# Performance work log

Measured on AMD Instinct MI355X. Metric: run time of the kernel, lower is better.

Reference implementation:

```python
import jax, jax.numpy as jnp
import numpy as np
from jax import lax

DIM = 1024
D_STATE = 64
D_CONV = 4
EXPAND = 2
HEADDIM = 64
D_INNER = EXPAND * DIM            # 2048
NHEADS = D_INNER // HEADDIM       # 32
NGROUPS = 1
CONV_DIM = D_INNER + 2 * NGROUPS * D_STATE      # 2176
D_IN_PROJ = 2 * D_INNER + 2 * NGROUPS * D_STATE + NHEADS  # 4256
BATCH, SEQLEN = 2, 4096
EPS = 1e-5


def setup_inputs() -> dict:
    key = jax.random.key(0)
    ks = jax.random.split(key, 10)
    X = jax.random.normal(ks[0], (BATCH, SEQLEN, DIM), dtype=jnp.float32)
    in_proj_w = jax.random.normal(ks[1], (D_IN_PROJ, DIM), dtype=jnp.float32) * 0.02
    conv_w = jax.random.normal(ks[2], (CONV_DIM, 1, D_CONV), dtype=jnp.float32) * 0.2
    conv_b = jax.random.normal(ks[3], (CONV_DIM,), dtype=jnp.float32) * 0.02
    dt_bias = jax.random.normal(ks[4], (NHEADS,), dtype=jnp.float32) * 0.5 - 2.0
    A_log = jnp.log(jax.random.uniform(ks[5], (NHEADS,), minval=1.0, maxval=16.0))
    D = jax.random.normal(ks[6], (NHEADS,), dtype=jnp.float32)
    norm_w = jnp.ones((D_INNER,), dtype=jnp.float32)
    out_proj_w = jax.random.normal(ks[7], (DIM, D_INNER), dtype=jnp.float32) * 0.02
    to_h_w = jax.random.normal(ks[8], (2 * DIM, DIM), dtype=jnp.float32) * 0.02
    return dict(X=X, in_proj_w=in_proj_w, conv_w=conv_w, conv_b=conv_b,
                dt_bias=dt_bias, A_log=A_log, D=D, norm_w=norm_w,
                out_proj_w=out_proj_w, to_h_w=to_h_w)


def _silu(x):
    return x * jax.nn.sigmoid(x)


def _mamba2(X, in_proj_w, conv_w, conv_b, dt_bias, A_log, D, norm_w, out_proj_w):
    Bsz, L, _ = X.shape
    zxbcdt = jnp.einsum('bld,ed->ble', X, in_proj_w)  # (B,L,D_IN_PROJ)
    z = zxbcdt[..., :D_INNER]
    xBC = zxbcdt[..., D_INNER:D_INNER + CONV_DIM]
    dt_raw = zxbcdt[..., D_INNER + CONV_DIM:]
    dt = jax.nn.softplus(dt_raw + dt_bias)  # (B,L,H)

    # causal depthwise conv over time, then silu
    xc = jnp.transpose(xBC, (0, 2, 1))                       # (B,C,L)
    xc = jnp.pad(xc, ((0, 0), (0, 0), (D_CONV - 1, 0)))
    xc = lax.conv_general_dilated(xc, conv_w, window_strides=(1,), padding='VALID',
                                  dimension_numbers=('NCH', 'OIH', 'NCH'),
                                  feature_group_count=CONV_DIM)
    xc = xc + conv_b[None, :, None]
    xBC = _silu(jnp.transpose(xc, (0, 2, 1)))                # (B,L,C)

    x = xBC[..., :D_INNER].reshape(Bsz, L, NHEADS, HEADDIM)  # (B,L,H,P)
    Bm = xBC[..., D_INNER:D_INNER + D_STATE]                 # (B,L,N) ngroups=1
    Cm = xBC[..., D_INNER + D_STATE:]                        # (B,L,N)

    A = -jnp.exp(A_log)                                      # (H,)

    def step(h, inp):
        dt_t, B_t, C_t, x_t = inp   # (B,H), (B,N), (B,N), (B,H,P)
        dA = jnp.exp(dt_t * A)                               # (B,H)
        h = h * dA[..., None, None] + jnp.einsum('bh,bhp,bn->bhpn', dt_t, x_t, B_t)
        y_t = jnp.einsum('bhpn,bn->bhp', h, C_t)
        return h, y_t

    h0 = jnp.zeros((Bsz, NHEADS, HEADDIM, D_STATE), dtype=X.dtype)
    xs = (jnp.moveaxis(dt, 1, 0), jnp.moveaxis(Bm, 1, 0),
          jnp.moveaxis(Cm, 1, 0), jnp.moveaxis(x, 1, 0))
    _, ys = lax.scan(step, h0, xs)                           # (L,B,H,P)
    y = jnp.moveaxis(ys, 0, 1) + x * D[None, None, :, None]  # skip term
    y = y.reshape(Bsz, L, D_INNER)

    # gated RMSNorm: rmsnorm(y * silu(z)) * weight
    y = y * _silu(z)
    y = y * lax.rsqrt(jnp.mean(y * y, axis=-1, keepdims=True) + EPS) * norm_w
    return jnp.einsum('bld,ed->ble', y, out_proj_w)          # (B,L,DIM)


def reference(X, in_proj_w, conv_w, conv_b, dt_bias, A_log, D, norm_w, out_proj_w, to_h_w):
    H = _mamba2(X, in_proj_w, conv_w, conv_b, dt_bias, A_log, D, norm_w, out_proj_w)
    HKV = jnp.einsum('bld,ed->ble', H, to_h_w)               # (B,L,2*DIM)
    HK, HV = HKV[..., :DIM], HKV[..., DIM:]
    return (HK, HV)
```

## Files before the change

### kernel.cpp

```cpp
#include <hip/hip_runtime.h>
#include <hip/hip_bf16.h>
#include <math.h>

#define B_       2
#define L_       4096
#define DIM_     1024
#define DINNER_  2048
#define DSTATE_  64
#define NH_      32
#define HD_      64
#define CONVDIM_ 2176
#define DIP_     4256
#define M_       (B_*L_)
#define XRW_     2208
#define NC_      64

typedef __attribute__((ext_vector_type(8))) short short8;
typedef __attribute__((ext_vector_type(4))) float floatx4;
typedef __hip_bfloat16 bf16;

__device__ __forceinline__ float bf2f(unsigned short u) {
    unsigned int v = ((unsigned int)u) << 16;
    return __builtin_bit_cast(float, v);
}
__device__ __forceinline__ unsigned short f2bf(float f) {
    unsigned int x = __builtin_bit_cast(unsigned int, f);
    unsigned int lsb = (x >> 16) & 1u;
    x += 0x7fffu + lsb;
    return (unsigned short)(x >> 16);
}
__device__ __forceinline__ void storeo(bf16* p, float v) {
    *reinterpret_cast<unsigned short*>(p) = f2bf(v);
}
__device__ __forceinline__ void storeo(float* p, float v) { *p = v; }

__device__ __forceinline__ void gl2lds16(const bf16* g, short* lds) {
    __builtin_amdgcn_global_load_lds(
        (const __attribute__((address_space(1))) void*)g,
        (__attribute__((address_space(3))) void*)lds, 16, 0, 0);
}

__global__ __launch_bounds__(256) void cast_f32_bf16_k(
    const float* __restrict__ src, bf16* __restrict__ dst)
{
    size_t i0 = ((size_t)blockIdx.x * 256 + threadIdx.x) * 8;
    uint4 a = *reinterpret_cast<const uint4*>(src + i0);
    uint4 b = *reinterpret_cast<const uint4*>(src + i0 + 4);
    unsigned int w0 = (unsigned int)f2bf(__builtin_bit_cast(float, a.x)) |
                      ((unsigned int)f2bf(__builtin_bit_cast(float, a.y)) << 16);
    unsigned int w1 = (unsigned int)f2bf(__builtin_bit_cast(float, a.z)) |
                      ((unsigned int)f2bf(__builtin_bit_cast(float, a.w)) << 16);
    unsigned int w2 = (unsigned int)f2bf(__builtin_bit_cast(float, b.x)) |
                      ((unsigned int)f2bf(__builtin_bit_cast(float, b.y)) << 16);
    unsigned int w3 = (unsigned int)f2bf(__builtin_bit_cast(float, b.z)) |
                      ((unsigned int)f2bf(__builtin_bit_cast(float, b.w)) << 16);
    *reinterpret_cast<uint4*>(reinterpret_cast<unsigned short*>(dst) + i0) =
        make_uint4(w0, w1, w2, w3);
}

template <typename TO>
__global__ __launch_bounds__(512, 2) void gemm256(
    const bf16* __restrict__ Ag, const bf16* __restrict__ Wg,
    TO* __restrict__ outA, TO* __restrict__ outB,
    int M, int N, int K, int split, int strideA, int strideB, int nbx)
{
    __shared__ short lds[65536];

    const int tid  = threadIdx.x;
    const int wave = tid >> 6;
    const int lane = tid & 63;
    const int ln   = lane & 15;
    const int quad = lane >> 4;
    const int wr   = wave >> 2;
    const int wc   = wave & 3;
    const int bh   = wc >> 1;
    const int wcl  = wc & 1;
    const int xorv = (ln & 7) << 4;

    int nwg  = gridDim.x;
    int orig = blockIdx.x;
    int wg   = ((nwg & 7) == 0) ? ((orig & 7) * (nwg >> 3) + (orig >> 3)) : orig;
    const int bx = wg % nbx;
    const int by = wg / nbx;
    const int m0 = by * 256;
    const int n0 = bx * 256;

    int lo0 = tid * 16;
    int lo1 = 8192 + tid * 16;
    int so0 = lo0 ^ (((lo0 >> 7) & 7) << 4);
    int so1 = lo1 ^ (((lo1 >> 7) & 7) << 4);
    const int srow0 = so0 >> 7, scol0 = (so0 & 127) >> 1;
    const int srow1 = so1 >> 7, scol1 = (so1 & 127) >> 1;

#define STG_A(bufb, h, kc) do {                                               \
    short* dst_ = &lds[((bufb)*2 + (h)) * 8192 + wave * 512];                 \
    gl2lds16(Ag + (size_t)(m0 + (h)*128 + srow0) * K + (kc) + scol0, dst_);   \
    gl2lds16(Ag + (size_t)(m0 + (h)*128 + srow1) * K + (kc) + scol1, dst_ + 4096); \
} while (0)
#define STG_B(bufb, h, kc) do {                                               \
    short* dst_ = &lds[32768 + ((bufb)*2 + (h)) * 8192 + wave * 512];         \
    gl2lds16(Wg + (size_t)(n0 + (h)*128 + srow0) * K + (kc) + scol0, dst_);   \
    gl2lds16(Wg + (size_t)(n0 + (h)*128 + srow1) * K + (kc) + scol1, dst_ + 4096); \
} while (0)

#define RD_A(qi) do {                                                         \
    const char* Ab_ = (const char*)&lds[(cur*2 + wr) * 8192];                 \
    _Pragma("unroll") for (int i = 0; i < 4; i++)                             \
    _Pragma("unroll") for (int ks = 0; ks < 2; ks++)                          \
        af[i][ks] = *reinterpret_cast<const short8*>(                         \
            Ab_ + ((((qi)*64 + i*16 + ln)*128 + ks*64 + quad*16) ^ xorv));    \
} while (0)
#define RD_B(qj, BV) do {                                                     \
    const char* Bb_ = (const char*)&lds[32768 + (cur*2 + bh) * 8192];         \
    _Pragma("unroll") for (int j = 0; j < 2; j++)                             \
    _Pragma("unroll") for (int ks = 0; ks < 2; ks++)                          \
        BV[j][ks] = *reinterpret_cast<const short8*>(                         \
            Bb_ + (((wcl*64 + (qj)*32 + j*16 + ln)*128 + ks*64 + quad*16) ^ xorv)); \
} while (0)

#define MMA(qi, qj, BV) do {                                                  \
    _Pragma("unroll") for (int i = 0; i < 4; i++)                             \
    _Pragma("unroll") for (int j = 0; j < 2; j++)                             \
    _Pragma("unroll") for (int ks = 0; ks < 2; ks++)                          \
        acc[(qi)*4+i][(qj)*2+j] = __builtin_amdgcn_mfma_f32_16x16x32_bf16(    \
            af[i][ks], BV[j][ks], acc[(qi)*4+i][(qj)*2+j], 0, 0, 0);          \
} while (0)

    floatx4 acc[8][4];
#pragma unroll
    for (int i = 0; i < 8; i++)
#pragma unroll
        for (int j = 0; j < 4; j++) acc[i][j] = (floatx4){0.f, 0.f, 0.f, 0.f};

    const int NT = K >> 6;

    STG_A(0, 0, 0); STG_A(0, 1, 0);
    STG_B(0, 0, 0); STG_B(0, 1, 0);
    asm volatile("s_waitcnt vmcnt(0)" ::: "memory");
    __builtin_amdgcn_s_barrier();
    __builtin_amdgcn_sched_barrier(0);

    short8 af[4][2], bf0[2][2], bf1[2][2];

    for (int t = 0; t < NT; ++t) {
        const int cur = t & 1, nxt = cur ^ 1;
        const int kc  = (t + 1) << 6;
        const bool pf = (t + 1 < NT);

        RD_A(0);
        RD_B(0, bf0);
        RD_B(1, bf1);

        if (pf) {
            STG_A(nxt, 0, kc); STG_A(nxt, 1, kc);
            STG_B(nxt, 0, kc); STG_B(nxt, 1, kc);
        }

        __builtin_amdgcn_s_setprio(1);
        MMA(0, 0, bf0);
        MMA(0, 1, bf1);
        RD_A(1);
        MMA(1, 1, bf1);
        MMA(1, 0, bf0);
        __builtin_amdgcn_s_setprio(0);

        if (pf) { asm volatile("s_waitcnt vmcnt(0)" ::: "memory"); }
        __builtin_amdgcn_s_barrier();
        __builtin_amdgcn_sched_barrier(0);
    }

#undef STG_A
#undef STG_B
#undef RD_A
#undef RD_B
#undef MMA

#pragma unroll
    for (int qi = 0; qi < 2; qi++)
#pragma unroll
    for (int i = 0; i < 4; i++)
#pragma unroll
    for (int qj = 0; qj < 2; qj++)
#pragma unroll
    for (int j = 0; j < 2; j++)
#pragma unroll
    for (int r = 0; r < 4; r++) {
        int grow = m0 + wr*128 + qi*64 + i*16 + quad*4 + r;
        int gcol = n0 + wc*64 + qj*32 + j*16 + ln;
        float v = acc[qi*4+i][qj*2+j][r];
        if (gcol < N) {
            if (gcol < split)
                storeo(outA + (size_t)grow * strideA + gcol, v);
            else
                storeo(outB + (size_t)grow * strideB + (gcol - split), v);
        }
    }
}

__global__ __launch_bounds__(256) void conv_all_k(
    const bf16* __restrict__ xr, const float* __restrict__ cw,
    const float* __restrict__ cb, bf16* __restrict__ xc)
{
    int idx = blockIdx.x * 256 + threadIdx.x;
    int row = idx / 272;
    int ch0 = (idx - row * 272) * 8;
    int t   = row & (L_ - 1);
    const unsigned short* xru = (const unsigned short*)xr;
    uint4 rv[4];
#pragma unroll
    for (int j = 0; j < 4; j++) {
        rv[j] = make_uint4(0u, 0u, 0u, 0u);
        if (t + j - 3 >= 0)
            rv[j] = *reinterpret_cast<const uint4*>(xru + (size_t)(row + j - 3) * XRW_ + ch0);
    }
    unsigned int ow[4];
#pragma unroll
    for (int pair = 0; pair < 4; pair++) {
        unsigned short o2[2];
#pragma unroll
        for (int k = 0; k < 2; k++) {
            int cc = pair * 2 + k;
            float a = cb[ch0 + cc];
#pragma unroll
            for (int j = 0; j < 4; j++) {
                unsigned int w32 = (&rv[j].x)[cc >> 1];
                unsigned short u = (cc & 1) ? (unsigned short)(w32 >> 16)
                                            : (unsigned short)(w32 & 0xffffu);
                a = fmaf(bf2f(u), cw[(ch0 + cc) * 4 + j], a);
            }
            o2[k] = f2bf(a / (1.f + __expf(-a)));
        }
        ow[pair] = (unsigned int)o2[0] | ((unsigned int)o2[1] << 16);
    }
    *reinterpret_cast<uint4*>((unsigned short*)xc + (size_t)row * CONVDIM_ + ch0) =
        make_uint4(ow[0], ow[1], ow[2], ow[3]);
}

__global__ __launch_bounds__(256) void dt_k(
    const bf16* __restrict__ xr, const float* __restrict__ dtb, float* __restrict__ dtf)
{
    int idx = blockIdx.x * 256 + threadIdx.x;
    int h  = idx & (NH_ - 1);
    int ml = idx >> 5;
    float v = bf2f(((const unsigned short*)xr)[(size_t)ml * XRW_ + 2176 + h]) + dtb[h];
    dtf[idx] = fmaxf(v, 0.f) + log1pf(__expf(-fabsf(v)));
}

__global__ __launch_bounds__(256) void chunk_intra_k(
    const bf16* __restrict__ xc, const float* __restrict__ dtf,
    const float* __restrict__ A_log, const float* __restrict__ Dp,
    bf16* __restrict__ Yg, float* __restrict__ Sg, float* __restrict__ Eg)
{
    __shared__ short Bst[64*72];
    __shared__ short Cst[64*72];
    __shared__ short xsM[64*72];
    __shared__ short xT [64*72];
    __shared__ short BwT[64*72];
    __shared__ float dts[64], cums[64], wS[64];

    const int tid  = threadIdx.x;
    const int bid  = blockIdx.x;
    const int h    = bid & 31;
    const int bc   = bid >> 5;
    const int c    = bc & 63;
    const int b    = bc >> 6;
    const int xch0 = h * 64;
    const unsigned short* xcu = (const unsigned short*)xc;

    const float Ah = -__expf(A_log[h]);
    const float Dh = Dp[h];

    for (int q = tid; q < 1536; q += 256) {
        int sel = q >> 9;
        int qq  = q & 511;
        int r = qq >> 3, c8 = (qq & 7) * 8;
        size_t ro = (size_t)(b * L_ + c * 64 + r) * CONVDIM_;
        if (sel == 0)
            *reinterpret_cast<uint4*>(&Bst[r*72 + c8]) =
                *reinterpret_cast<const uint4*>(xcu + ro + 2048 + c8);
        else if (sel == 1)
            *reinterpret_cast<uint4*>(&Cst[r*72 + c8]) =
                *reinterpret_cast<const uint4*>(xcu + ro + 2112 + c8);
        else
            *reinterpret_cast<uint4*>(&xsM[r*72 + c8]) =
                *reinterpret_cast<const uint4*>(xcu + ro + xch0 + c8);
    }
    if (tid < 64) dts[tid] = dtf[(size_t)(b * L_ + c * 64 + tid) * NH_ + h];
    __syncthreads();

    if (tid == 0) {
        float cc = 0.f;
        for (int t = 0; t < 64; t++) { cc += dts[t] * Ah; cums[t] = cc; }
    }
    __syncthreads();
    if (tid < 64) wS[tid] = __expf(cums[63] - cums[tid]) * dts[tid];
    if (tid == 0) Eg[bid] = __expf(cums[63]);
    __syncthreads();

    for (int q = tid; q < 4096; q += 256) {
        int s = q & 63, ch = q >> 6;
        xT [ch*72 + s] = xsM[s*72 + ch];
        BwT[ch*72 + s] = (short)f2bf(bf2f((unsigned short)Bst[s*72 + ch]) * wS[s]);
    }
    __syncthreads();

    const int wave = tid >> 6, lane = tid & 63;
    const int ln = lane & 15, quad = lane >> 4;
    const int wm = (wave >> 1) * 32, wn = (wave & 1) * 32;

    floatx4 accG[2][2];
#pragma unroll
    for (int i = 0; i < 2; i++)
#pragma unroll
        for (int j = 0; j < 2; j++) accG[i][j] = (floatx4){0.f,0.f,0.f,0.f};
#pragma unroll
    for (int kk = 0; kk < 64; kk += 32) {
        short8 af[2], bfv[2];
#pragma unroll
        for (int i = 0; i < 2; i++)
            af[i] = *reinterpret_cast<const short8*>(&Cst[(wm + i*16 + ln)*72 + kk + quad*8]);
#pragma unroll
        for (int j = 0; j < 2; j++)
            bfv[j] = *reinterpret_cast<const short8*>(&Bst[(wn + j*16 + ln)*72 + kk + quad*8]);
#pragma unroll
        for (int i = 0; i < 2; i++)
#pragma unroll
            for (int j = 0; j < 2; j++)
                accG[i][j] = __builtin_amdgcn_mfma_f32_16x16x32_bf16(af[i], bfv[j], accG[i][j], 0,0,0);
    }
    __syncthreads();
#pragma unroll
    for (int i = 0; i < 2; i++)
#pragma unroll
        for (int j = 0; j < 2; j++)
#pragma unroll
            for (int r = 0; r < 4; r++) {
                int t = wm + i*16 + quad*4 + r;
                int s = wn + j*16 + ln;
                float v = (s <= t) ? __expf(cums[t] - cums[s]) * dts[s] * accG[i][j][r] : 0.f;
                xsM[t*72 + s] = (short)f2bf(v);
            }
    __syncthreads();

    floatx4 accY[2][2];
#pragma unroll
    for (int i = 0; i < 2; i++)
#pragma unroll
        for (int j = 0; j < 2; j++) accY[i][j] = (floatx4){0.f,0.f,0.f,0.f};
#pragma unroll
    for (int kk = 0; kk < 64; kk += 32) {
        short8 af[2], bfv[2];
#pragma unroll
        for (int i = 0; i < 2; i++)
            af[i] = *reinterpret_cast<const short8*>(&xsM[(wm + i*16 + ln)*72 + kk + quad*8]);
#pragma unroll
        for (int j = 0; j < 2; j++)
            bfv[j] = *reinterpret_cast<const short8*>(&xT[(wn + j*16 + ln)*72 + kk + quad*8]);
#pragma unroll
        for (int i = 0; i < 2; i++)
#pragma unroll
            for (int j = 0; j < 2; j++)
                accY[i][j] = __builtin_amdgcn_mfma_f32_16x16x32_bf16(af[i], bfv[j], accY[i][j], 0,0,0);
    }
    unsigned short* Yu = (unsigned short*)Yg;
#pragma unroll
    for (int i = 0; i < 2; i++)
#pragma unroll
        for (int j = 0; j < 2; j++)
#pragma unroll
            for (int r = 0; r < 4; r++) {
                int t = wm + i*16 + quad*4 + r;
                int p = wn + j*16 + ln;
                float yv = accY[i][j][r] + Dh * bf2f((unsigned short)xT[p*72 + t]);
                Yu[(size_t)(b*L_ + c*64 + t)*DINNER_ + xch0 + p] = f2bf(yv);
            }

    floatx4 accS[2][2];
#pragma unroll
    for (int i = 0; i < 2; i++)
#pragma unroll
        for (int j = 0; j < 2; j++) accS[i][j] = (floatx4){0.f,0.f,0.f,0.f};
#pragma unroll
    for (int kk = 0; kk < 64; kk += 32) {
        short8 af[2], bfv[2];
#pragma unroll
        for (int i = 0; i < 2; i++)
            af[i] = *reinterpret_cast<const short8*>(&xT[(wm + i*16 + ln)*72 + kk + quad*8]);
#pragma unroll
        for (int j = 0; j < 2; j++)
            bfv[j] = *reinterpret_cast<const short8*>(&BwT[(wn + j*16 + ln)*72 + kk + quad*8]);
#pragma unroll
        for (int i = 0; i < 2; i++)
#pragma unroll
            for (int j = 0; j < 2; j++)
                accS[i][j] = __builtin_amdgcn_mfma_f32_16x16x32_bf16(af[i], bfv[j], accS[i][j], 0,0,0);
    }
#pragma unroll
    for (int i = 0; i < 2; i++)
#pragma unroll
        for (int j = 0; j < 2; j++)
#pragma unroll
            for (int r = 0; r < 4; r++) {
                int p = wm + i*16 + quad*4 + r;
                int n = wn + j*16 + ln;
                Sg[(size_t)bid * 4096 + p*64 + n] = accS[i][j][r];
            }
}

__global__ __launch_bounds__(256) void chunk_state_k(
    float* __restrict__ Sg, const float* __restrict__ Eg)
{
    int g  = blockIdx.x * 1024 + threadIdx.x * 4;
    int bh = g >> 12;
    int b  = bh >> 5, h = bh & 31;
    int e  = g & 4095;
    float4 run = make_float4(0.f, 0.f, 0.f, 0.f);
    for (int c = 0; c < NC_; c++) {
        int bid = (b * 64 + c) * 32 + h;
        size_t idx = (size_t)bid * 4096 + e;
        float4 s = *reinterpret_cast<float4*>(&Sg[idx]);
        float  E = Eg[bid];
        *reinterpret_cast<float4*>(&Sg[idx]) = run;
        run.x = run.x * E + s.x;
        run.y = run.y * E + s.y;
        run.z = run.z * E + s.z;
        run.w = run.w * E + s.w;
    }
}

__global__ __launch_bounds__(256) void chunk_inter_k(
    const bf16* __restrict__ xc, const float* __restrict__ Sg,
    const float* __restrict__ dtf, const float* __restrict__ A_log,
    bf16* __restrict__ Yg)
{
    __shared__ short Cst[64*72];
    __shared__ short hpT[64*72];
    __shared__ float dts[64], cums[64], wcumL[64];

    const int tid = threadIdx.x;
    const int bid = blockIdx.x;
    const int h   = bid & 31;
    const int bc  = bid >> 5;
    const int c   = bc & 63;
    const int b   = bc >> 6;
    const unsigned short* xcu = (const unsigned short*)xc;

    const float Ah = -__expf(A_log[h]);

    for (int q = tid; q < 512; q += 256) {
        int r = q >> 3, c8 = (q & 7) * 8;
        *reinterpret_cast<uint4*>(&Cst[r*72 + c8]) =
            *reinterpret_cast<const uint4*>(xcu + (size_t)(b*L_ + c*64 + r)*CONVDIM_ + 2112 + c8);
    }
    for (int q = tid; q < 1024; q += 256) {
        int p = q >> 4, n4 = (q & 15) * 4;
        float4 v = *reinterpret_cast<const float4*>(&Sg[(size_t)bid * 4096 + p*64 + n4]);
        unsigned int lo = (unsigned int)f2bf(v.x) | ((unsigned int)f2bf(v.y) << 16);
        unsigned int hi = (unsigned int)f2bf(v.z) | ((unsigned int)f2bf(v.w) << 16);
        *reinterpret_cast<uint2*>(&hpT[p*72 + n4]) = make_uint2(lo, hi);
    }
    if (tid < 64) dts[tid] = dtf[(size_t)(b*L_ + c*64 + tid) * NH_ + h];
    __syncthreads();
    if (tid == 0) {
        float cc = 0.f;
        for (int t = 0; t < 64; t++) { cc += dts[t] * Ah; cums[t] = cc; }
    }
    __syncthreads();
    if (tid < 64) wcumL[tid] = __expf(cums[tid]);
    __syncthreads();

    const int wave = tid >> 6, lane = tid & 63;
    const int ln = lane & 15, quad = lane >> 4;
    const int wm = (wave >> 1) * 32, wn = (wave & 1) * 32;

    floatx4 acc[2][2];
#pragma unroll
    for (int i = 0; i < 2; i++)
#pragma unroll
        for (int j = 0; j < 2; j++) acc[i][j] = (floatx4){0.f,0.f,0.f,0.f};
#pragma unroll
    for (int kk = 0; kk < 64; kk += 32) {
        short8 af[2], bfv[2];
#pragma unroll
        for (int i = 0; i < 2; i++)
            af[i] = *reinterpret_cast<const short8*>(&Cst[(wm + i*16 + ln)*72 + kk + quad*8]);
#pragma unroll
        for (int j = 0; j < 2; j++)
            bfv[j] = *reinterpret_cast<const short8*>(&hpT[(wn + j*16 + ln)*72 + kk + quad*8]);
#pragma unroll
        for (int i = 0; i < 2; i++)
#pragma unroll
            for (int j = 0; j < 2; j++)
                acc[i][j] = __builtin_amdgcn_mfma_f32_16x16x32_bf16(af[i], bfv[j], acc[i][j], 0,0,0);
    }
    unsigned short* Yu = (unsigned short*)Yg;
#pragma unroll
    for (int i = 0; i < 2; i++)
#pragma unroll
        for (int j = 0; j < 2; j++)
#pragma unroll
            for (int r = 0; r < 4; r++) {
                int t = wm + i*16 + quad*4 + r;
                int p = wn + j*16 + ln;
                size_t idx = (size_t)(b*L_ + c*64 + t)*DINNER_ + h*64 + p;
                float yv = bf2f(Yu[idx]) + wcumL[t] * acc[i][j][r];
                Yu[idx] = f2bf(yv);
            }
}

__global__ __launch_bounds__(256) void gate_norm_k(
    bf16* __restrict__ y, const bf16* __restrict__ zbuf, const float* __restrict__ nw)
{
    __shared__ float red[4];
    int row = blockIdx.x;
    int tid = threadIdx.x;
    unsigned short* yy = (unsigned short*)y;
    const unsigned short* zz = (const unsigned short*)zbuf;

    uint4 yv = *reinterpret_cast<uint4*>(&yy[(size_t)row * DINNER_ + tid * 8]);
    uint4 zv = *reinterpret_cast<const uint4*>(&zz[(size_t)row * DINNER_ + tid * 8]);
    unsigned int yw[4] = {yv.x, yv.y, yv.z, yv.w};
    unsigned int zw[4] = {zv.x, zv.y, zv.z, zv.w};
    float g[8];
    float ss = 0.f;
#pragma unroll
    for (int q = 0; q < 4; q++) {
        float y0 = bf2f((unsigned short)(yw[q] & 0xffffu)), y1 = bf2f((unsigned short)(yw[q] >> 16));
        float z0 = bf2f((unsigned short)(zw[q] & 0xffffu)), z1 = bf2f((unsigned short)(zw[q] >> 16));
        float g0 = y0 * (z0 / (1.f + __expf(-z0)));
        float g1 = y1 * (z1 / (1.f + __expf(-z1)));
        g[q * 2] = g0; g[q * 2 + 1] = g1;
        ss += g0 * g0 + g1 * g1;
    }
#pragma unroll
    for (int o = 1; o < 64; o <<= 1) ss += __shfl_xor(ss, o);
    if ((tid & 63) == 0) red[tid >> 6] = ss;
    __syncthreads();
    float tot = red[0] + red[1] + red[2] + red[3];
    float rinv = rsqrtf(tot * (1.f / DINNER_) + 1e-5f);

    unsigned int ow[4];
#pragma unroll
    for (int q = 0; q < 4; q++) {
        float w0 = nw[tid * 8 + q * 2];
        float w1 = nw[tid * 8 + q * 2 + 1];
        unsigned short o0 = f2bf(g[q * 2] * rinv * w0);
        unsigned short o1 = f2bf(g[q * 2 + 1] * rinv * w1);
        ow[q] = (unsigned int)o0 | ((unsigned int)o1 << 16);
    }
    *reinterpret_cast<uint4*>(&yy[(size_t)row * DINNER_ + tid * 8]) =
        make_uint4(ow[0], ow[1], ow[2], ow[3]);
}


extern "C" void kernel_launch(void* const* d_in, const int* in_sizes, int n_in,
                              void* d_out, int out_size, void* d_ws, size_t ws_size,
                              hipStream_t stream)
{
    const float* X    = (const float*)d_in[0];
    const float* Wip  = (const float*)d_in[1];
    const float* cw   = (const float*)d_in[2];
    const float* cb   = (const float*)d_in[3];
    const float* dtb  = (const float*)d_in[4];
    const float* Alog = (const float*)d_in[5];
    const float* Dp   = (const float*)d_in[6];
    const float* nw   = (const float*)d_in[7];
    const float* Wop  = (const float*)d_in[8];
    const float* Wth  = (const float*)d_in[9];
    float* out = (float*)d_out;

    char* ws = (char*)d_ws;
    bf16*  zbuf = (bf16*) (ws);
    bf16*  Wopb = (bf16*) (ws);
    bf16*  Wthb = (bf16*) (ws + 4194304);
    bf16*  xr   = (bf16*) (ws + 33554432);
    bf16*  Yg   = (bf16*) (ws + 33554432);
    bf16*  xc   = (bf16*) (ws + 69730304);
    bf16*  Xb   = (bf16*) (ws + 69730304);
    bf16*  Wipb = (bf16*) (ws + 69730304 + 16777216);
    bf16*  Hbuf = (bf16*) (ws + 69730304);
    float* dtf  = (float*)(ws + 105381888);
    float* Eg   = (float*)(ws + 106430464);
    float* Sg   = (float*)d_out;

    dim3 blk(256);
    dim3 blk512(512);

    cast_f32_bf16_k<<<(M_ * DIM_) / 2048, blk, 0, stream>>>(X, Xb);
    cast_f32_bf16_k<<<(DIP_ * DIM_) / 2048, blk, 0, stream>>>(Wip, Wipb);

    gemm256<bf16><<<dim3(17 * 32), blk512, 0, stream>>>(
        Xb, Wipb, zbuf, xr, M_, DIP_, DIM_, DINNER_, DINNER_, XRW_, 17);

    dt_k<<<(M_ * NH_) / 256, blk, 0, stream>>>(xr, dtb, dtf);
    conv_all_k<<<(M_ * 272) / 256, blk, 0, stream>>>(xr, cw, cb, xc);

    chunk_intra_k<<<B_ * NC_ * NH_, blk, 0, stream>>>(
        xc, dtf, Alog, Dp, Yg, Sg, Eg);
    chunk_state_k<<<256, blk, 0, stream>>>(Sg, Eg);
    chunk_inter_k<<<B_ * NC_ * NH_, blk, 0, stream>>>(xc, Sg, dtf, Alog, Yg);

    gate_norm_k<<<M_, blk, 0, stream>>>(Yg, zbuf, nw);

    cast_f32_bf16_k<<<(DIM_ * DINNER_) / 2048, blk, 0, stream>>>(Wop, Wopb);
    cast_f32_bf16_k<<<(DINNER_ * DIM_) / 2048, blk, 0, stream>>>(Wth, Wthb);

    gemm256<bf16><<<dim3(4 * 32), blk512, 0, stream>>>(
        Yg, Wopb, Hbuf, Hbuf, M_, DIM_, DINNER_, DIM_, DIM_, DIM_, 4);

    gemm256<float><<<dim3(8 * 32), blk512, 0, stream>>>(
        Hbuf, Wthb, out, out + (size_t)M_ * DIM_, M_, DINNER_, DIM_, DIM_, DIM_, DIM_, 8);
}
```

Baseline: 472.5 us.

## Fold out_proj and to_h weights into one matrix before the final GEMM

Uses associativity to precompute a combined 2048x2048 weight, Wc = to_h_w @ out_proj_w, in bf16. A new cast-transpose kernel and a simple 128x128 MFMA GEMM build it, so the two chained activation GEMMs become one GEMM with K=2048. This removes the intermediate H buffer write and read plus one large GEMM launch. The total activation FLOPs stay the same, and it adds a small weight GEMM plus different bf16 rounding, since H is no longer quantised but Wc is.

Result: no change. 467.7 us (-1.0%).

```diff
diff --git a/kernel.cpp b/kernel.cpp
--- a/kernel.cpp
+++ b/kernel.cpp
@@ -56,6 +56,103 @@
                       ((unsigned int)f2bf(__builtin_bit_cast(float, b.w)) << 16);
     *reinterpret_cast<uint4*>(reinterpret_cast<unsigned short*>(dst) + i0) =
         make_uint4(w0, w1, w2, w3);
+}
+
+__global__ __launch_bounds__(256) void cast_transpose_k(
+    const float* __restrict__ src, bf16* __restrict__ dst, int R, int C)
+{
+    __shared__ unsigned short t[64][72];
+    int nct = C >> 6;
+    int r0 = (blockIdx.x / nct) << 6;
+    int c0 = (blockIdx.x % nct) << 6;
+    int tr = threadIdx.x >> 2;
+    int tc = (threadIdx.x & 3) << 4;
+    const float* s = src + (size_t)(r0 + tr) * C + c0 + tc;
+#pragma unroll
+    for (int k = 0; k < 16; k += 4) {
+        float4 v = *reinterpret_cast<const float4*>(s + k);
+        t[tr][tc + k + 0] = f2bf(v.x);
+        t[tr][tc + k + 1] = f2bf(v.y);
+        t[tr][tc + k + 2] = f2bf(v.z);
+        t[tr][tc + k + 3] = f2bf(v.w);
+    }
+    __syncthreads();
+    unsigned short* d = (unsigned short*)dst + (size_t)(c0 + tr) * R + r0 + tc;
+    unsigned int ww[8];
+#pragma unroll
+    for (int q = 0; q < 8; q++)
+        ww[q] = (unsigned int)t[tc + 2*q][tr] | ((unsigned int)t[tc + 2*q + 1][tr] << 16);
+    *reinterpret_cast<uint4*>(d)     = make_uint4(ww[0], ww[1], ww[2], ww[3]);
+    *reinterpret_cast<uint4*>(d + 8) = make_uint4(ww[4], ww[5], ww[6], ww[7]);
+}
+
+template <typename TO>
+__global__ __launch_bounds__(256) void gemm_bt16(
+    const bf16* __restrict__ A, const bf16* __restrict__ W,
+    TO* __restrict__ outA, TO* __restrict__ outB,
+    int M, int N, int K, int split, int strideA, int strideB)
+{
+    __shared__ short As[128*64];
+    __shared__ short Ws[128*64];
+    const int tid  = threadIdx.x;
+    const int m0   = blockIdx.y * 128;
+    const int n0   = blockIdx.x * 128;
+    const int wave = tid >> 6;
+    const int lane = tid & 63;
+    const int wm   = (wave >> 1) * 64;
+    const int wn   = (wave & 1) * 64;
+    const int ln   = lane & 15;
+    const int quad = lane >> 4;
+    const int lr   = lane >> 3;
+    const int lc   = (lane & 7) * 8;
+
+    floatx4 acc[4][4];
+#pragma unroll
+    for (int i = 0; i < 4; i++)
+#pragma unroll
+        for (int j = 0; j < 4; j++) acc[i][j] = (floatx4){0.f, 0.f, 0.f, 0.f};
+
+    for (int k0 = 0; k0 < K; k0 += 64) {
+#pragma unroll
+        for (int it = 0; it < 4; it++) {
+            int ig = wave * 4 + it;
+            gl2lds16(A + (size_t)(m0 + ig * 8 + lr) * K + k0 + lc, &As[ig * 512]);
+            gl2lds16(W + (size_t)(n0 + ig * 8 + lr) * K + k0 + lc, &Ws[ig * 512]);
+        }
+        __syncthreads();
+#pragma unroll
+        for (int kk = 0; kk < 64; kk += 32) {
+            short8 af[4], bfv[4];
+#pragma unroll
+            for (int i = 0; i < 4; i++)
+                af[i] = *reinterpret_cast<const short8*>(&As[(wm + i * 16 + ln) * 64 + kk + quad * 8]);
+#pragma unroll
+            for (int j = 0; j < 4; j++)
+                bfv[j] = *reinterpret_cast<const short8*>(&Ws[(wn + j * 16 + ln) * 64 + kk + quad * 8]);
+#pragma unroll
+            for (int i = 0; i < 4; i++)
+#pragma unroll
+                for (int j = 0; j < 4; j++)
+                    acc[i][j] = __builtin_amdgcn_mfma_f32_16x16x32_bf16(af[i], bfv[j], acc[i][j], 0, 0, 0);
+        }
+        __syncthreads();
+    }
+
+#pragma unroll
+    for (int i = 0; i < 4; i++)
+#pragma unroll
+        for (int j = 0; j < 4; j++)
+#pragma unroll
+            for (int r = 0; r < 4; r++) {
+                int grow = m0 + wm + i * 16 + quad * 4 + r;
+                int gcol = n0 + wn + j * 16 + ln;
+                if (gcol < N) {
+                    if (gcol < split)
+                        storeo(outA + (size_t)grow * strideA + gcol, acc[i][j][r]);
+                    else
+                        storeo(outB + (size_t)grow * strideB + (gcol - split), acc[i][j][r]);
+                }
+            }
 }
 
 template <typename TO>
@@ -571,14 +668,14 @@
 
     char* ws = (char*)d_ws;
     bf16*  zbuf = (bf16*) (ws);
-    bf16*  Wopb = (bf16*) (ws);
+    bf16*  WopT = (bf16*) (ws);
     bf16*  Wthb = (bf16*) (ws + 4194304);
+    bf16*  Wc   = (bf16*) (ws + 8388608);
     bf16*  xr   = (bf16*) (ws + 33554432);
     bf16*  Yg   = (bf16*) (ws + 33554432);
     bf16*  xc   = (bf16*) (ws + 69730304);
     bf16*  Xb   = (bf16*) (ws + 69730304);
     bf16*  Wipb = (bf16*) (ws + 69730304 + 16777216);
-    bf16*  Hbuf = (bf16*) (ws + 69730304);
     float* dtf  = (float*)(ws + 105381888);
     float* Eg   = (float*)(ws + 106430464);
     float* Sg   = (float*)d_out;
@@ -602,12 +699,11 @@
 
     gate_norm_k<<<M_, blk, 0, stream>>>(Yg, zbuf, nw);
 
-    cast_f32_bf16_k<<<(DIM_ * DINNER_) / 2048, blk, 0, stream>>>(Wop, Wopb);
+    cast_transpose_k<<<(1024/64) * (2048/64), blk, 0, stream>>>(Wop, WopT, 1024, 2048);
     cast_f32_bf16_k<<<(DINNER_ * DIM_) / 2048, blk, 0, stream>>>(Wth, Wthb);
-
-    gemm256<bf16><<<dim3(4 * 32), blk512, 0, stream>>>(
-        Yg, Wopb, Hbuf, Hbuf, M_, DIM_, DINNER_, DIM_, DIM_, DIM_, 4);
+    gemm_bt16<bf16><<<dim3(16, 16), blk, 0, stream>>>(
+        Wthb, WopT, Wc, Wc, DINNER_, DINNER_, DIM_, DINNER_, DINNER_, DINNER_);
 
     gemm256<float><<<dim3(8 * 32), blk512, 0, stream>>>(
-        Hbuf, Wthb, out, out + (size_t)M_ * DIM_, M_, DINNER_, DIM_, DIM_, DIM_, DIM_, 8);
-}
+        Yg, Wc, out, out + (size_t)M_ * DIM_, M_, DINNER_, DINNER_, DIM_, DIM_, DIM_, 8);
+}
```
